# Kernel optimization log

Hardware: AMD Instinct MI355X
Metric: run time of the kernel (lower is better)

The kernel has to match this reference:

```python
import jax, jax.numpy as jnp
import numpy as np

B, H, S, W, F = 16, 4, 8, 256, 16


def setup_inputs() -> dict:
    key = jax.random.key(0)
    kx, kk = jax.random.split(key)
    x = jax.random.normal(kx, (B, S, W, F), dtype=jnp.float32)
    kernel = jax.random.normal(kk, (H, S, S, W), dtype=jnp.float32)
    return {"x": x, "kernel": kernel}


def reference(x, kernel):
    # kernel: [H, S, S, W]; x: [B, S, W, F]
    Hh, Ss, _, Ww = kernel.shape
    r = jnp.arange(Ww)
    # stacked[h,x,y,j,i] = roll(kernel, shifts=j+1)[i] = kernel[(i-(j+1)) % W]
    idx = (r[None, :] - (r[:, None] + 1)) % Ww          # [W(row=j), W(col=i)]
    stacked = kernel[..., idx]                            # [H,S,S,W,W]
    # torch.tril over last two dims: keep col i <= row j
    tri = (r[None, :] <= r[:, None])                      # [W,W]
    stacked = jnp.where(tri, stacked, jnp.zeros((), dtype=stacked.dtype))
    # masked triangular time-mix contraction
    out = jnp.einsum('hxyji,bxif->bhxyjf', stacked, x)    # [B,H,S,S,W,F]
    base = jnp.arange(1, Ww + 1, dtype=out.dtype).reshape(1, 1, 1, 1, Ww, 1)
    out = out / base
    # transform_x: on diagonal series (x==y) roll time dim by 1, zero first step
    diag_mod = jnp.roll(out, 1, axis=4)
    not_first = (r != 0).reshape(1, 1, 1, 1, Ww, 1)
    diag_mod = diag_mod * not_first.astype(out.dtype)
    eye = jnp.eye(Ss, dtype=bool).reshape(1, 1, Ss, Ss, 1, 1)
    return jnp.where(eye, diag_mod, out)
```

## Files before the change

kernel.cpp:

```cpp
#include <hip/hip_runtime.h>
#include <hip/hip_bf16.h>

typedef short short8 __attribute__((ext_vector_type(8)));
typedef float f32x4 __attribute__((ext_vector_type(4)));

union FragAB { unsigned long long l[2]; int i[4]; short8 v; };

__global__ __launch_bounds__(256, 3)
void k_fused(const float* __restrict__ x,
             const float* __restrict__ kern,
             float* __restrict__ out)
{
    __shared__ __align__(16) ushort Xts[64 * 264];
    __shared__ __align__(8)  ushort wforL[4][336];
    __shared__ float rtab[256];

    const int blk = blockIdx.x;
    const int hy = blk & 31;
    const int sx = (blk >> 5) & 7;
    const int nt = blk >> 8;
    const int h = hy >> 3, sy = hy & 7;
    const int diag = (sx == sy) ? 1 : 0;
    const int t = threadIdx.x;

    {
        const float* krow = kern + ((h * 8 + sx) * 8 + sy) * 256;
        #pragma unroll
        for (int s = 0; s < 4; ++s) {
            #pragma unroll
            for (int pass = 0; pass < 2; ++pass) {
                int q = t + pass * 256;
                if (q < 336) {
                    int src = q - s;
                    float v = (src >= 0 && src < 256) ? krow[src] : 0.0f;
                    __hip_bfloat16 hv = __float2bfloat16(v);
                    wforL[s][q] = reinterpret_cast<ushort&>(hv);
                }
            }
        }
    }
    {
        int denom = t + 1 - diag;
        rtab[t] = (denom > 0) ? (1.0f / (float)denom) : 0.0f;
    }
    {
        const float4* xbase = reinterpret_cast<const float4*>(x);
        #pragma unroll
        for (int it = 0; it < 8; ++it) {
            int id = it * 256 + t;
            int fq = id & 3;
            int k2 = (id >> 2) & 127;
            int bl = id >> 9;
            const float4* rowp = xbase + ((size_t)((nt * 4 + bl) * 8 + sx)) * 1024;
            float4 a = rowp[(2 * k2) * 4 + fq];
            float4 cq = rowp[(2 * k2 + 1) * 4 + fq];
            #pragma unroll
            for (int e = 0; e < 4; ++e) {
                float va = (&a.x)[e], vb = (&cq.x)[e];
                __hip_bfloat16 ha = __float2bfloat16(va);
                __hip_bfloat16 hb = __float2bfloat16(vb);
                uint u = (uint)reinterpret_cast<ushort&>(ha) |
                         ((uint)reinterpret_cast<ushort&>(hb) << 16);
                int row = bl * 16 + fq * 4 + e;
                *reinterpret_cast<uint*>(reinterpret_cast<char*>(Xts) + row * 528 + k2 * 4) = u;
            }
        }
    }
    __syncthreads();

    const int lane = t & 63, wid = t >> 6;
    const int laneM = lane & 15, laneG = lane >> 4;
    const int wp  = wid >> 1;
    const int par = wid & 1;

    const char* XtsB = reinterpret_cast<const char*>(Xts);
    const char* WB = reinterpret_cast<const char*>(wforL);
    const int abyte = (32 * wp + laneM) * 528 + laneG * 16;

    const int w00 = 255 + diag - 16 * par - laneM + 8 * laneG;
    const int s = (laneM - diag + 1 - 16 * par) & 3;
    const int bBw = s * 674 + 2 * w00;

    f32x4 acc[8][2];
    #pragma unroll
    for (int g = 0; g < 8; ++g)
        #pragma unroll
        for (int m = 0; m < 2; ++m)
            acc[g][m] = (f32x4){0.0f, 0.0f, 0.0f, 0.0f};

    #pragma unroll
    for (int st = 0; st < 8; ++st) {
        const int kc = 32 * st;
        FragAB af[2];
        #pragma unroll
        for (int m = 0; m < 2; ++m) {
            const int4 raw = *reinterpret_cast<const int4*>(
                XtsB + abyte + m * 8448 + kc * 2);
            af[m].i[0] = raw.x; af[m].i[1] = raw.y;
            af[m].i[2] = raw.z; af[m].i[3] = raw.w;
        }
        #pragma unroll
        for (int g = 0; g < 8; ++g) {
            if (g >= st) {
                FragAB bf;
                const char* p = WB + bBw - 64 * g + kc * 2;
                bf.l[0] = *reinterpret_cast<const unsigned long long*>(p);
                bf.l[1] = *reinterpret_cast<const unsigned long long*>(p + 8);
                #pragma unroll
                for (int m = 0; m < 2; ++m)
                    acc[g][m] = __builtin_amdgcn_mfma_f32_16x16x32_bf16(
                        af[m].v, bf.v, acc[g][m], 0, 0, 0);
            }
            if (g == st) {
                const int j = 32 * g + 16 * par + laneM;
                const float rt = rtab[j];
                #pragma unroll
                for (int m = 0; m < 2; ++m) {
                    const int b_ = nt * 4 + 2 * wp + m;
                    float* dst = out
                        + (((size_t)(b_ * 4 + h) * 8 + sx) * 8 + sy) * 4096
                        + (size_t)j * 16 + laneG * 4;
                    f32x4 v = acc[g][m] * rt;
                    __builtin_nontemporal_store(v, reinterpret_cast<f32x4*>(dst));
                }
            }
        }
    }
}

extern "C" void kernel_launch(void* const* d_in, const int* in_sizes, int n_in,
                              void* d_out, int out_size, void* d_ws, size_t ws_size,
                              hipStream_t stream) {
    const float* x    = (const float*)d_in[0];
    const float* kern = (const float*)d_in[1];
    float* out = (float*)d_out;

    k_fused<<<1024, 256, 0, stream>>>(x, kern, out);
}
```

Measured before the change: 20.69 us.

## Halve batch tile per block and double grid for higher occupancy

Each block now handles 2 batch rows instead of 4, and the grid doubles from 1024 to 2048 blocks. Each wave keeps one MFMA accumulator set instead of two, and launch bounds rise to 6 blocks per SIMD budget. The smaller register and shared-memory footprint is meant to let more waves stay resident, so the output-write-bound kernel hides memory latency better. In exchange, every block redundantly rebuilds the kernel-row table and reciprocal table, and each loaded A fragment is reused for fewer MFMAs.

New measurement: 27.50 us. 32.9% more time.

```diff
diff --git a/kernel.cpp b/kernel.cpp
--- a/kernel.cpp
+++ b/kernel.cpp
@@ -6,19 +6,19 @@
 
 union FragAB { unsigned long long l[2]; int i[4]; short8 v; };
 
-__global__ __launch_bounds__(256, 3)
+__global__ __launch_bounds__(256, 6)
 void k_fused(const float* __restrict__ x,
              const float* __restrict__ kern,
              float* __restrict__ out)
 {
-    __shared__ __align__(16) ushort Xts[64 * 264];
+    __shared__ __align__(16) ushort Xts[32 * 264];
     __shared__ __align__(8)  ushort wforL[4][336];
     __shared__ float rtab[256];
 
     const int blk = blockIdx.x;
     const int hy = blk & 31;
     const int sx = (blk >> 5) & 7;
-    const int nt = blk >> 8;
+    const int np = blk >> 8;
     const int h = hy >> 3, sy = hy & 7;
     const int diag = (sx == sy) ? 1 : 0;
     const int t = threadIdx.x;
@@ -46,12 +46,12 @@
     {
         const float4* xbase = reinterpret_cast<const float4*>(x);
         #pragma unroll
-        for (int it = 0; it < 8; ++it) {
+        for (int it = 0; it < 4; ++it) {
             int id = it * 256 + t;
             int fq = id & 3;
             int k2 = (id >> 2) & 127;
             int bl = id >> 9;
-            const float4* rowp = xbase + ((size_t)((nt * 4 + bl) * 8 + sx)) * 1024;
+            const float4* rowp = xbase + ((size_t)((np * 2 + bl) * 8 + sx)) * 1024;
             float4 a = rowp[(2 * k2) * 4 + fq];
             float4 cq = rowp[(2 * k2 + 1) * 4 + fq];
             #pragma unroll
@@ -75,29 +75,28 @@
 
     const char* XtsB = reinterpret_cast<const char*>(Xts);
     const char* WB = reinterpret_cast<const char*>(wforL);
-    const int abyte = (32 * wp + laneM) * 528 + laneG * 16;
+    const int abyte = (16 * wp + laneM) * 528 + laneG * 16;
+    const int b_ = np * 2 + wp;
+    float* const oblk = out + (((size_t)(b_ * 4 + h) * 8 + sx) * 8 + sy) * 4096
+                        + laneG * 4;
 
     const int w00 = 255 + diag - 16 * par - laneM + 8 * laneG;
-    const int s = (laneM - diag + 1 - 16 * par) & 3;
+    const int s = (laneM - diag + 1) & 3;
     const int bBw = s * 674 + 2 * w00;
 
-    f32x4 acc[8][2];
+    f32x4 acc[8];
     #pragma unroll
     for (int g = 0; g < 8; ++g)
-        #pragma unroll
-        for (int m = 0; m < 2; ++m)
-            acc[g][m] = (f32x4){0.0f, 0.0f, 0.0f, 0.0f};
+        acc[g] = (f32x4){0.0f, 0.0f, 0.0f, 0.0f};
 
     #pragma unroll
     for (int st = 0; st < 8; ++st) {
         const int kc = 32 * st;
-        FragAB af[2];
-        #pragma unroll
-        for (int m = 0; m < 2; ++m) {
-            const int4 raw = *reinterpret_cast<const int4*>(
-                XtsB + abyte + m * 8448 + kc * 2);
-            af[m].i[0] = raw.x; af[m].i[1] = raw.y;
-            af[m].i[2] = raw.z; af[m].i[3] = raw.w;
+        FragAB af;
+        {
+            const int4 raw = *reinterpret_cast<const int4*>(XtsB + abyte + kc * 2);
+            af.i[0] = raw.x; af.i[1] = raw.y;
+            af.i[2] = raw.z; af.i[3] = raw.w;
         }
         #pragma unroll
         for (int g = 0; g < 8; ++g) {
@@ -106,23 +105,14 @@
                 const char* p = WB + bBw - 64 * g + kc * 2;
                 bf.l[0] = *reinterpret_cast<const unsigned long long*>(p);
                 bf.l[1] = *reinterpret_cast<const unsigned long long*>(p + 8);
-                #pragma unroll
-                for (int m = 0; m < 2; ++m)
-                    acc[g][m] = __builtin_amdgcn_mfma_f32_16x16x32_bf16(
-                        af[m].v, bf.v, acc[g][m], 0, 0, 0);
+                acc[g] = __builtin_amdgcn_mfma_f32_16x16x32_bf16(
+                    af.v, bf.v, acc[g], 0, 0, 0);
             }
             if (g == st) {
                 const int j = 32 * g + 16 * par + laneM;
-                const float rt = rtab[j];
-                #pragma unroll
-                for (int m = 0; m < 2; ++m) {
-                    const int b_ = nt * 4 + 2 * wp + m;
-                    float* dst = out
-                        + (((size_t)(b_ * 4 + h) * 8 + sx) * 8 + sy) * 4096
-                        + (size_t)j * 16 + laneG * 4;
-                    f32x4 v = acc[g][m] * rt;
-                    __builtin_nontemporal_store(v, reinterpret_cast<f32x4*>(dst));
-                }
+                f32x4 v = acc[g] * rtab[j];
+                __builtin_nontemporal_store(
+                    v, reinterpret_cast<f32x4*>(oblk + (size_t)j * 16));
             }
         }
     }
@@ -135,5 +125,5 @@
     const float* kern = (const float*)d_in[1];
     float* out = (float*)d_out;
 
-    k_fused<<<1024, 256, 0, stream>>>(x, kern, out);
+    k_fused<<<2048, 256, 0, stream>>>(x, kern, out);
 }
```
